# Optimization experiments

Measured on AMD Instinct MI355X. Metric: run time of the kernel, lower is better.

The kernel has to match this reference:

```python
import jax, jax.numpy as jnp
import numpy as np

EPS = 1e-5  # BatchNorm eps; BN applied in eval mode with running_mean=0, running_var=1


def conv1x1(x, w, b=None):
    # x: [B,C,H,W], w: [O,C] -> [B,O,H,W]
    y = jnp.einsum('bchw,oc->bohw', x, w)
    if b is not None:
        y = y + b[None, :, None, None]
    return y


def bn_eval(x, gamma, beta):
    # running_mean=0, running_var=1
    scale = gamma / jnp.sqrt(1.0 + EPS)
    return x * scale[None, :, None, None] + beta[None, :, None, None]


def glnl_forward(x, mask, wt_nl, bt_nl, wp_nl, bp_nl, wt_l, bt_l, wp_l, bp_l,
                 wg_nl, bg_nl, wg_l, bg_l, wW, bW, gW, betaW, wWl, gWl, betaWl):
    B, C, H, W = x.shape
    I = wt_nl.shape[0]
    N = H * W

    # non-local branch score [B,N,N]
    th_nl = conv1x1(x, wt_nl, bt_nl).reshape(B, I, N)
    ph_nl = conv1x1(x, wp_nl, bp_nl).reshape(B, I, N)
    score_nl = jax.nn.softmax(jnp.einsum('bin,bim->bnm', th_nl, ph_nl), axis=-1)

    # local branch: mask-gated projections, score [B,N,N]
    m = mask.reshape(B, 1, N)
    th_l = conv1x1(x, wt_l, bt_l).reshape(B, I, N) * m
    ph_l = conv1x1(x, wp_l, bp_l).reshape(B, I, N) * m
    score_l = jax.nn.softmax(jnp.einsum('bin,bim->bnm', th_l, ph_l), axis=-1)

    # value projections [B,I,N]
    g_nl = conv1x1(x, wg_nl, bg_nl).reshape(B, I, N)
    g_l = conv1x1(x, wg_l, bg_l).reshape(B, I, N)

    # attention aggregation -> [B,I,H,W]
    y_nl = jnp.einsum('bnm,bim->bin', score_nl, g_nl).reshape(B, I, H, W)
    y_l = jnp.einsum('bnm,bim->bin', score_l, g_l).reshape(B, I, H, W)

    # W_local: conv1x1 (no bias) -> ReLU -> BN
    y_l = bn_eval(jax.nn.relu(conv1x1(y_l, wWl)), gWl, betaWl)

    y = y_nl + y_l
    # W: conv1x1 -> ReLU -> BN, then residual
    W_y = bn_eval(jax.nn.relu(conv1x1(y, wW, bW)), gW, betaW)
    return W_y + x


def setup_inputs() -> dict:
    key = jax.random.key(0)
    ks = jax.random.split(key, 20)
    B, C, I, H, W = 4, 128, 64, 64, 64
    s = 0.02
    inp = {
        'x': jax.random.normal(ks[0], (B, C, H, W), jnp.float32),
        'mask': (jax.random.uniform(ks[1], (B, 1, H, W)) > 0.5).astype(jnp.float32),
        'wt_nl': jax.random.normal(ks[2], (I, C)) * s, 'bt_nl': jnp.zeros((I,)),
        'wp_nl': jax.random.normal(ks[3], (I, C)) * s, 'bp_nl': jnp.zeros((I,)),
        'wt_l': jax.random.normal(ks[4], (I, C)) * s, 'bt_l': jnp.zeros((I,)),
        'wp_l': jax.random.normal(ks[5], (I, C)) * s, 'bp_l': jnp.zeros((I,)),
        'wg_nl': jax.random.normal(ks[6], (I, C)) * s, 'bg_nl': jnp.zeros((I,)),
        'wg_l': jax.random.normal(ks[7], (I, C)) * s, 'bg_l': jnp.zeros((I,)),
        'wW': jax.random.normal(ks[8], (C, I)) * s, 'bW': jnp.zeros((C,)),
        'gW': jnp.ones((C,)), 'betaW': jnp.zeros((C,)),
        'wWl': jax.random.normal(ks[9], (I, I)) * s,
        'gWl': jnp.ones((I,)), 'betaWl': jnp.zeros((I,)),
    }
    return inp


def reference(x, mask, wt_nl, bt_nl, wp_nl, bp_nl, wt_l, bt_l, wp_l, bp_l,
              wg_nl, bg_nl, wg_l, bg_l, wW, bW, gW, betaW, wWl, gWl, betaWl):
    return glnl_forward(x, mask, wt_nl, bt_nl, wp_nl, bp_nl, wt_l, bt_l, wp_l, bp_l,
                        wg_nl, bg_nl, wg_l, bg_l, wW, bW, gW, betaW, wWl, gWl, betaWl)
```

## Files before the change

### kernel.cpp

```cpp
#include <hip/hip_runtime.h>

typedef unsigned short u16;
typedef __attribute__((ext_vector_type(8))) short short8;
typedef __attribute__((ext_vector_type(4))) float floatx4;

#define MFMA16(a, b, c) __builtin_amdgcn_mfma_f32_16x16x32_bf16((a), (b), (c), 0, 0, 0)

#define SZ_P ((size_t)4 * 64 * 4096)

__device__ __forceinline__ float bf2f(u16 u) {
    union { unsigned int i; float f; } v; v.i = ((unsigned int)u) << 16; return v.f;
}
__device__ __forceinline__ u16 f2bf(float f) {
    union { float f; unsigned int i; } v; v.f = f;
    unsigned int r = v.i + 0x7fffu + ((v.i >> 16) & 1u);
    return (u16)(r >> 16);
}
__device__ __forceinline__ short8 pack8(const float* __restrict__ p) {
    short8 r;
#pragma unroll
    for (int j = 0; j < 8; ++j) r[j] = (short)f2bf(p[j]);
    return r;
}
__device__ __forceinline__ unsigned int pk2(float a, float b) {
    union { float f; unsigned int u; } x, y; x.f = a; y.f = b;
    return (x.u >> 16) | (y.u & 0xffff0000u);
}

__global__ __launch_bounds__(256) void k_proj(
    const float* __restrict__ x, const float* __restrict__ mask,
    const float* __restrict__ wq0, const float* __restrict__ bq0,
    const float* __restrict__ wk0, const float* __restrict__ bk0,
    const float* __restrict__ wv0, const float* __restrict__ bv0,
    const float* __restrict__ wq1, const float* __restrict__ bq1,
    const float* __restrict__ wk1, const float* __restrict__ bk1,
    const float* __restrict__ wv1, const float* __restrict__ bv1,
    u16* __restrict__ q0, u16* __restrict__ k0, u16* __restrict__ v0,
    u16* __restrict__ q1, u16* __restrict__ k1, u16* __restrict__ v1)
{
    __shared__ __align__(16) u16 xt_s[64 * 136];
    const int n0 = blockIdx.x * 64, b = blockIdx.y, br = blockIdx.z;
    const float* wq = br ? wq1 : wq0;  const float* bq = br ? bq1 : bq0;
    const float* wk = br ? wk1 : wk0;  const float* bk = br ? bk1 : bk0;
    const float* wv = br ? wv1 : wv0;  const float* bv = br ? bv1 : bv0;
    u16* q = br ? q1 : q0;  u16* k = br ? k1 : k0;  u16* v = br ? v1 : v0;

    const int t = threadIdx.x, w = t >> 6, lane = t & 63;
    const int quad = lane >> 4, l15 = lane & 15;
    const float* xb = x + ((size_t)b << 19);

    for (int idx = t; idx < 8192; idx += 256) {
        const int c = idx >> 6, n = idx & 63;
        xt_s[n * 136 + c] = f2bf(xb[((size_t)c << 12) + n0 + n]);
    }
    __syncthreads();

    short8 ax[4];
#pragma unroll
    for (int cc = 0; cc < 4; ++cc)
        ax[cc] = *(const short8*)&xt_s[(w * 16 + l15) * 136 + quad * 8 + cc * 32];

    float mv[4] = {1.f, 1.f, 1.f, 1.f};
    if (br) {
#pragma unroll
        for (int r = 0; r < 4; ++r)
            mv[r] = mask[((size_t)b << 12) + n0 + w * 16 + quad * 4 + r];
    }

#pragma unroll
    for (int qk = 0; qk < 2; ++qk) {
        const float* wsel = qk ? wk : wq;
        const float* bb = qk ? bk : bq;
        u16* o = qk ? k : q;
#pragma unroll
        for (int ns = 0; ns < 4; ++ns) {
            floatx4 acc = {0.f, 0.f, 0.f, 0.f};
            const float* wp = wsel + (ns * 16 + l15) * 128 + quad * 8;
#pragma unroll
            for (int cc = 0; cc < 4; ++cc)
                acc = MFMA16(ax[cc], pack8(wp + cc * 32), acc);
            const float bias_i = bb[ns * 16 + l15];
#pragma unroll
            for (int r = 0; r < 4; ++r) {
                const float val = (acc[r] + bias_i) * mv[r];
                o[((size_t)b << 18) + (size_t)(n0 + w * 16 + quad * 4 + r) * 64
                  + ns * 16 + l15] = f2bf(val);
            }
        }
    }

    short8 aw[4];
#pragma unroll
    for (int cc = 0; cc < 4; ++cc)
        aw[cc] = pack8(wv + (w * 16 + l15) * 128 + quad * 8 + cc * 32);
    float bvr[4];
#pragma unroll
    for (int r = 0; r < 4; ++r) bvr[r] = bv[w * 16 + quad * 4 + r];
#pragma unroll
    for (int ns = 0; ns < 4; ++ns) {
        floatx4 acc = {0.f, 0.f, 0.f, 0.f};
#pragma unroll
        for (int cc = 0; cc < 4; ++cc)
            acc = MFMA16(aw[cc],
                *(const short8*)&xt_s[(ns * 16 + l15) * 136 + quad * 8 + cc * 32], acc);
#pragma unroll
        for (int r = 0; r < 4; ++r) {
            v[((size_t)b << 18) + ((size_t)(w * 16 + quad * 4 + r) << 12)
              + n0 + ns * 16 + l15] = f2bf(acc[r] + bvr[r]);
        }
    }
}

__global__ __launch_bounds__(256) void k_flash(
    const u16* __restrict__ Q0, const u16* __restrict__ K0,
    const u16* __restrict__ V0,
    const u16* __restrict__ Q1, const u16* __restrict__ K1,
    const u16* __restrict__ V1,
    u16* __restrict__ num, float* __restrict__ den)
{
    __shared__ __align__(16) u16 kt_s[2][64 * 72];
    __shared__ __align__(16) u16 vt_s[2][64 * 72];
    __shared__ __align__(16) u16 p_s[4 * 32 * 72];

    const int flat = blockIdx.x;
    const int g = flat & 15, tile = flat >> 4;
    const int b = g >> 2, z = g & 3;
    const int br = z >> 1, sp = z & 1;
    const int qb = tile * 128;
    const size_t base = ((size_t)b << 18);
    const u16* Q = (br ? Q1 : Q0) + base;
    const u16* K = (br ? K1 : K0) + base;
    const u16* V = (br ? V1 : V0) + base;
    u16* numo = num + (size_t)z * SZ_P + base;
    float* deno = den + z * 16384 + b * 4096;

    const int t = threadIdx.x, w = t >> 6, lane = t & 63;
    const int quad = lane >> 4, l15 = lane & 15;
    const int pw = w * 32 * 72;

    const int r0 = t >> 3, r1 = (t + 256) >> 3, cg8 = (t & 7) * 8;
    const u16* Kp0 = K + (size_t)r0 * 64 + cg8;
    const u16* Kp1 = K + (size_t)r1 * 64 + cg8;
    const u16* Vp0 = V + ((size_t)r0 << 12) + cg8;
    const u16* Vp1 = V + ((size_t)r1 << 12) + cg8;
    const int lk0 = r0 * 72 + cg8, lk1 = r1 * 72 + cg8;

    short8 aq[2][2];
#pragma unroll
    for (int t2 = 0; t2 < 2; ++t2)
#pragma unroll
        for (int s = 0; s < 2; ++s)
            aq[t2][s] = *(const short8*)(Q + (size_t)(qb + w * 32 + t2 * 16 + l15) * 64
                                         + s * 32 + quad * 8);

    floatx4 oacc[4][2];
#pragma unroll
    for (int it = 0; it < 4; ++it)
#pragma unroll
        for (int t2 = 0; t2 < 2; ++t2) oacc[it][t2] = (floatx4){0.f, 0.f, 0.f, 0.f};
    float dacc[2] = {0.f, 0.f};

    const int roff = tile & 31;
    const int m_beg = sp * 2048;

    {
        const int m0 = m_beg + (roff << 6);
        *(short8*)&kt_s[0][lk0] = *(const short8*)(Kp0 + (size_t)m0 * 64);
        *(short8*)&kt_s[0][lk1] = *(const short8*)(Kp1 + (size_t)m0 * 64);
        *(short8*)&vt_s[0][lk0] = *(const short8*)(Vp0 + m0);
        *(short8*)&vt_s[0][lk1] = *(const short8*)(Vp1 + m0);
    }

    for (int j = 0; j < 32; ++j) {
        const int cur = j & 1;
        const int mn = m_beg + (((roff + j + 1) & 31) << 6);
        short8 pk0v = *(const short8*)(Kp0 + (size_t)mn * 64);
        short8 pk1v = *(const short8*)(Kp1 + (size_t)mn * 64);
        short8 pv0v = *(const short8*)(Vp0 + mn);
        short8 pv1v = *(const short8*)(Vp1 + mn);
        __syncthreads();

#pragma unroll
        for (int mt = 0; mt < 4; ++mt) {
            const u16* kp = &kt_s[cur][(mt * 16 + l15) * 72 + quad * 8];
            const short8 ka0 = *(const short8*)kp;
            const short8 ka1 = *(const short8*)(kp + 32);
#pragma unroll
            for (int t2 = 0; t2 < 2; ++t2) {
                floatx4 acc = {0.f, 0.f, 0.f, 0.f};
                acc = MFMA16(ka0, aq[t2][0], acc);
                acc = MFMA16(ka1, aq[t2][1], acc);
                const float e0 = __expf(acc[0]), e1 = __expf(acc[1]);
                const float e2 = __expf(acc[2]), e3 = __expf(acc[3]);
                dacc[t2] += (e0 + e1) + (e2 + e3);
                *(uint2*)&p_s[pw + (t2 * 16 + l15) * 72 + mt * 16 + quad * 4] =
                    make_uint2(pk2(e0, e1), pk2(e2, e3));
            }
        }

        short8 pb2[2][2];
#pragma unroll
        for (int t2 = 0; t2 < 2; ++t2)
#pragma unroll
            for (int s = 0; s < 2; ++s)
                pb2[t2][s] = *(const short8*)&p_s[pw + (t2 * 16 + l15) * 72 + s * 32 + quad * 8];
#pragma unroll
        for (int it = 0; it < 4; ++it) {
            const u16* vp = &vt_s[cur][(it * 16 + l15) * 72 + quad * 8];
            const short8 va0 = *(const short8*)vp;
            const short8 va1 = *(const short8*)(vp + 32);
#pragma unroll
            for (int t2 = 0; t2 < 2; ++t2) {
                oacc[it][t2] = MFMA16(va0, pb2[t2][0], oacc[it][t2]);
                oacc[it][t2] = MFMA16(va1, pb2[t2][1], oacc[it][t2]);
            }
        }

        *(short8*)&kt_s[cur ^ 1][lk0] = pk0v;
        *(short8*)&kt_s[cur ^ 1][lk1] = pk1v;
        *(short8*)&vt_s[cur ^ 1][lk0] = pv0v;
        *(short8*)&vt_s[cur ^ 1][lk1] = pv1v;
    }

#pragma unroll
    for (int t2 = 0; t2 < 2; ++t2) {
        float d = dacc[t2];
        d += __shfl_xor(d, 16, 64);
        d += __shfl_xor(d, 32, 64);
        if (quad == 0) deno[qb + w * 32 + t2 * 16 + l15] = d;
    }

#pragma unroll
    for (int it = 0; it < 4; ++it)
#pragma unroll
        for (int t2 = 0; t2 < 2; ++t2) {
            *(uint2*)&p_s[pw + (t2 * 16 + l15) * 72 + it * 16 + quad * 4] =
                make_uint2(pk2(oacc[it][t2][0], oacc[it][t2][1]),
                           pk2(oacc[it][t2][2], oacc[it][t2][3]));
        }
    __syncthreads();
#pragma unroll
    for (int ch = t; ch < 1024; ch += 256) {
        const int row = ch >> 3, cg = ch & 7;
        *(short8*)(numo + (size_t)(qb + row) * 64 + cg * 8) =
            *(const short8*)&p_s[(row >> 5) * 2304 + (row & 31) * 72 + cg * 8];
    }
}

__global__ __launch_bounds__(256) void k_epi(
    const u16* __restrict__ num, const float* __restrict__ den,
    const float* __restrict__ wWl, const float* __restrict__ gWl,
    const float* __restrict__ betaWl,
    const float* __restrict__ wW, const float* __restrict__ bW,
    const float* __restrict__ gW, const float* __restrict__ betaW,
    const float* __restrict__ x, float* __restrict__ out)
{
    __shared__ __align__(16) u16 yl_s[16 * 72];
    __shared__ __align__(16) u16 ynl_s[16 * 72];
    __shared__ __align__(16) u16 yy_s[16 * 72];
    const int b = blockIdx.y, n0 = blockIdx.x * 16;
    const int t = threadIdx.x, w = t >> 6, lane = t & 63;
    const int quad = lane >> 4, l15 = lane & 15;
    const size_t ybase = ((size_t)b << 18) + (size_t)n0 * 64;

    if (t < 128) {
        const int row = t >> 3, cg = t & 7;
        const float dn = den[b * 4096 + n0 + row] + den[16384 + b * 4096 + n0 + row];
        const float dl = den[32768 + b * 4096 + n0 + row] + den[49152 + b * 4096 + n0 + row];
        const float inl = 1.0f / dn, ilo = 1.0f / dl;
        const short8 a0 = *(const short8*)(num + ybase + row * 64 + cg * 8);
        const short8 a1 = *(const short8*)(num + SZ_P + ybase + row * 64 + cg * 8);
        const short8 c0 = *(const short8*)(num + 2 * SZ_P + ybase + row * 64 + cg * 8);
        const short8 c1 = *(const short8*)(num + 3 * SZ_P + ybase + row * 64 + cg * 8);
        short8 ynl8, yl8;
#pragma unroll
        for (int j = 0; j < 8; ++j) {
            ynl8[j] = (short)f2bf((bf2f((u16)a0[j]) + bf2f((u16)a1[j])) * inl);
            yl8[j]  = (short)f2bf((bf2f((u16)c0[j]) + bf2f((u16)c1[j])) * ilo);
        }
        *(short8*)&ynl_s[row * 72 + cg * 8] = ynl8;
        *(short8*)&yl_s[row * 72 + cg * 8] = yl8;
    }
    __syncthreads();
    const float rsq = rsqrtf(1.0f + 1e-5f);

    {
        const short8 a0 = pack8(wWl + (w * 16 + l15) * 64 + quad * 8);
        const short8 a1 = pack8(wWl + (w * 16 + l15) * 64 + 32 + quad * 8);
        float sc[4], bt[4];
#pragma unroll
        for (int r = 0; r < 4; ++r) {
            const int io = w * 16 + quad * 4 + r;
            sc[r] = gWl[io] * rsq;
            bt[r] = betaWl[io];
        }
        floatx4 acc = {0.f, 0.f, 0.f, 0.f};
        const u16* bp_ = &yl_s[l15 * 72 + quad * 8];
        acc = MFMA16(a0, *(const short8*)bp_, acc);
        acc = MFMA16(a1, *(const short8*)(bp_ + 32), acc);
#pragma unroll
        for (int r = 0; r < 4; ++r) {
            const int io = w * 16 + quad * 4 + r;
            float val = fmaxf(acc[r], 0.f) * sc[r] + bt[r];
            val += bf2f(ynl_s[l15 * 72 + io]);
            yy_s[l15 * 72 + io] = f2bf(val);
        }
    }
    __syncthreads();

#pragma unroll
    for (int rb = 0; rb < 2; ++rb) {
        const int c0 = rb * 64 + w * 16;
        const short8 a0 = pack8(wW + (c0 + l15) * 64 + quad * 8);
        const short8 a1 = pack8(wW + (c0 + l15) * 64 + 32 + quad * 8);
        float bs[4], sc[4], bt[4];
#pragma unroll
        for (int r = 0; r < 4; ++r) {
            const int c = c0 + quad * 4 + r;
            bs[r] = bW[c];
            sc[r] = gW[c] * rsq;
            bt[r] = betaW[c];
        }
        floatx4 acc = {0.f, 0.f, 0.f, 0.f};
        const u16* bp_ = &yy_s[l15 * 72 + quad * 8];
        acc = MFMA16(a0, *(const short8*)bp_, acc);
        acc = MFMA16(a1, *(const short8*)(bp_ + 32), acc);
#pragma unroll
        for (int r = 0; r < 4; ++r) {
            const int c = c0 + quad * 4 + r;
            float val = fmaxf(acc[r] + bs[r], 0.f) * sc[r] + bt[r];
            const size_t xi = ((size_t)b << 19) + ((size_t)c << 12) + n0 + l15;
            out[xi] = val + x[xi];
        }
    }
}

extern "C" void kernel_launch(void* const* d_in, const int* in_sizes, int n_in,
                              void* d_out, int out_size, void* d_ws, size_t ws_size,
                              hipStream_t stream) {
    const float* x      = (const float*)d_in[0];
    const float* mask   = (const float*)d_in[1];
    const float* wt_nl  = (const float*)d_in[2];  const float* bt_nl = (const float*)d_in[3];
    const float* wp_nl  = (const float*)d_in[4];  const float* bp_nl = (const float*)d_in[5];
    const float* wt_l   = (const float*)d_in[6];  const float* bt_l  = (const float*)d_in[7];
    const float* wp_l   = (const float*)d_in[8];  const float* bp_l  = (const float*)d_in[9];
    const float* wg_nl  = (const float*)d_in[10]; const float* bg_nl = (const float*)d_in[11];
    const float* wg_l   = (const float*)d_in[12]; const float* bg_l  = (const float*)d_in[13];
    const float* wW     = (const float*)d_in[14]; const float* bW    = (const float*)d_in[15];
    const float* gW     = (const float*)d_in[16]; const float* betaW = (const float*)d_in[17];
    const float* wWl    = (const float*)d_in[18]; const float* gWl   = (const float*)d_in[19];
    const float* betaWl = (const float*)d_in[20];

    u16* ws  = (u16*)d_ws;
    u16* q0  = ws;
    u16* k0  = q0 + SZ_P;
    u16* v0  = k0 + SZ_P;
    u16* q1  = v0 + SZ_P;
    u16* k1  = q1 + SZ_P;
    u16* v1  = k1 + SZ_P;
    u16* num = v1 + SZ_P;
    float* den = (float*)(num + 4 * SZ_P);

    k_proj<<<dim3(64, 4, 2), 256, 0, stream>>>(x, mask,
        wt_nl, bt_nl, wp_nl, bp_nl, wg_nl, bg_nl,
        wt_l,  bt_l,  wp_l,  bp_l,  wg_l,  bg_l,
        q0, k0, v0, q1, k1, v1);
    k_flash<<<dim3(512), 256, 0, stream>>>(q0, k0, v0, q1, k1, v1, num, den);
    k_epi<<<dim3(256, 4), 256, 0, stream>>>(num, den, wWl, gWl, betaWl,
                                            wW, bW, gW, betaW, x, (float*)d_out);
}
```

Measured before the change: 189.7 us.

## Split key range four ways with 512-thread flash blocks and exp2 softmax

The flash kernel now uses 512-thread blocks covering 256 query rows each. The key dimension is split into four partitions instead of two, and each iteration loads one K/V chunk per thread. The epilogue sums four partial numerators and denominators per branch, and the workspace grows to hold eight partial buffers. Q is pre-scaled by log2(e) in the projection kernel so the inner loop can use exp2f instead of __expf. This trades extra partial-sum traffic and workspace for shorter per-block loops and more warps per block sharing each K/V tile.

```diff
diff --git a/kernel.cpp b/kernel.cpp
--- a/kernel.cpp
+++ b/kernel.cpp
@@ -5,6 +5,7 @@
 typedef __attribute__((ext_vector_type(4))) float floatx4;
 
 #define MFMA16(a, b, c) __builtin_amdgcn_mfma_f32_16x16x32_bf16((a), (b), (c), 0, 0, 0)
+#define LOG2E 1.44269504088896340736f
 
 #define SZ_P ((size_t)4 * 64 * 4096)
 
@@ -72,6 +73,7 @@
         const float* wsel = qk ? wk : wq;
         const float* bb = qk ? bk : bq;
         u16* o = qk ? k : q;
+        const float qscale = qk ? 1.0f : LOG2E;
 #pragma unroll
         for (int ns = 0; ns < 4; ++ns) {
             floatx4 acc = {0.f, 0.f, 0.f, 0.f};
@@ -82,7 +84,7 @@
             const float bias_i = bb[ns * 16 + l15];
 #pragma unroll
             for (int r = 0; r < 4; ++r) {
-                const float val = (acc[r] + bias_i) * mv[r];
+                const float val = (acc[r] + bias_i) * mv[r] * qscale;
                 o[((size_t)b << 18) + (size_t)(n0 + w * 16 + quad * 4 + r) * 64
                   + ns * 16 + l15] = f2bf(val);
             }
@@ -111,7 +113,7 @@
     }
 }
 
-__global__ __launch_bounds__(256) void k_flash(
+__global__ __launch_bounds__(512, 4) void k_flash(
     const u16* __restrict__ Q0, const u16* __restrict__ K0,
     const u16* __restrict__ V0,
     const u16* __restrict__ Q1, const u16* __restrict__ K1,
@@ -120,13 +122,13 @@
 {
     __shared__ __align__(16) u16 kt_s[2][64 * 72];
     __shared__ __align__(16) u16 vt_s[2][64 * 72];
-    __shared__ __align__(16) u16 p_s[4 * 32 * 72];
+    __shared__ __align__(16) u16 p_s[8 * 32 * 72];
 
     const int flat = blockIdx.x;
-    const int g = flat & 15, tile = flat >> 4;
-    const int b = g >> 2, z = g & 3;
-    const int br = z >> 1, sp = z & 1;
-    const int qb = tile * 128;
+    const int g = flat & 31, tile = flat >> 5;
+    const int b = g >> 3, br = (g >> 2) & 1, sp = g & 3;
+    const int z = br * 4 + sp;
+    const int qb = tile * 256;
     const size_t base = ((size_t)b << 18);
     const u16* Q = (br ? Q1 : Q0) + base;
     const u16* K = (br ? K1 : K0) + base;
@@ -138,12 +140,10 @@
     const int quad = lane >> 4, l15 = lane & 15;
     const int pw = w * 32 * 72;
 
-    const int r0 = t >> 3, r1 = (t + 256) >> 3, cg8 = (t & 7) * 8;
+    const int r0 = t >> 3, cg8 = (t & 7) * 8;
     const u16* Kp0 = K + (size_t)r0 * 64 + cg8;
-    const u16* Kp1 = K + (size_t)r1 * 64 + cg8;
     const u16* Vp0 = V + ((size_t)r0 << 12) + cg8;
-    const u16* Vp1 = V + ((size_t)r1 << 12) + cg8;
-    const int lk0 = r0 * 72 + cg8, lk1 = r1 * 72 + cg8;
+    const int lk0 = r0 * 72 + cg8;
 
     short8 aq[2][2];
 #pragma unroll
@@ -160,24 +160,20 @@
         for (int t2 = 0; t2 < 2; ++t2) oacc[it][t2] = (floatx4){0.f, 0.f, 0.f, 0.f};
     float dacc[2] = {0.f, 0.f};
 
-    const int roff = tile & 31;
-    const int m_beg = sp * 2048;
+    const int roff = tile & 15;
+    const int m_beg = sp * 1024;
 
     {
         const int m0 = m_beg + (roff << 6);
         *(short8*)&kt_s[0][lk0] = *(const short8*)(Kp0 + (size_t)m0 * 64);
-        *(short8*)&kt_s[0][lk1] = *(const short8*)(Kp1 + (size_t)m0 * 64);
         *(short8*)&vt_s[0][lk0] = *(const short8*)(Vp0 + m0);
-        *(short8*)&vt_s[0][lk1] = *(const short8*)(Vp1 + m0);
-    }
-
-    for (int j = 0; j < 32; ++j) {
+    }
+
+    for (int j = 0; j < 16; ++j) {
         const int cur = j & 1;
-        const int mn = m_beg + (((roff + j + 1) & 31) << 6);
-        short8 pk0v = *(const short8*)(Kp0 + (size_t)mn * 64);
-        short8 pk1v = *(const short8*)(Kp1 + (size_t)mn * 64);
-        short8 pv0v = *(const short8*)(Vp0 + mn);
-        short8 pv1v = *(const short8*)(Vp1 + mn);
+        const int mn = m_beg + (((roff + j + 1) & 15) << 6);
+        short8 pkv = *(const short8*)(Kp0 + (size_t)mn * 64);
+        short8 pvv = *(const short8*)(Vp0 + mn);
         __syncthreads();
 
 #pragma unroll
@@ -190,8 +186,8 @@
                 floatx4 acc = {0.f, 0.f, 0.f, 0.f};
                 acc = MFMA16(ka0, aq[t2][0], acc);
                 acc = MFMA16(ka1, aq[t2][1], acc);
-                const float e0 = __expf(acc[0]), e1 = __expf(acc[1]);
-                const float e2 = __expf(acc[2]), e3 = __expf(acc[3]);
+                const float e0 = exp2f(acc[0]), e1 = exp2f(acc[1]);
+                const float e2 = exp2f(acc[2]), e3 = exp2f(acc[3]);
                 dacc[t2] += (e0 + e1) + (e2 + e3);
                 *(uint2*)&p_s[pw + (t2 * 16 + l15) * 72 + mt * 16 + quad * 4] =
                     make_uint2(pk2(e0, e1), pk2(e2, e3));
@@ -216,10 +212,8 @@
             }
         }
 
-        *(short8*)&kt_s[cur ^ 1][lk0] = pk0v;
-        *(short8*)&kt_s[cur ^ 1][lk1] = pk1v;
-        *(short8*)&vt_s[cur ^ 1][lk0] = pv0v;
-        *(short8*)&vt_s[cur ^ 1][lk1] = pv1v;
+        *(short8*)&kt_s[cur ^ 1][lk0] = pkv;
+        *(short8*)&vt_s[cur ^ 1][lk0] = pvv;
     }
 
 #pragma unroll
@@ -240,7 +234,7 @@
         }
     __syncthreads();
 #pragma unroll
-    for (int ch = t; ch < 1024; ch += 256) {
+    for (int ch = t; ch < 2048; ch += 512) {
         const int row = ch >> 3, cg = ch & 7;
         *(short8*)(numo + (size_t)(qb + row) * 64 + cg * 8) =
             *(const short8*)&p_s[(row >> 5) * 2304 + (row & 31) * 72 + cg * 8];
@@ -265,18 +259,29 @@
 
     if (t < 128) {
         const int row = t >> 3, cg = t & 7;
-        const float dn = den[b * 4096 + n0 + row] + den[16384 + b * 4096 + n0 + row];
-        const float dl = den[32768 + b * 4096 + n0 + row] + den[49152 + b * 4096 + n0 + row];
+        float dn = 0.f, dl = 0.f;
+#pragma unroll
+        for (int sp = 0; sp < 4; ++sp) {
+            dn += den[sp * 16384 + b * 4096 + n0 + row];
+            dl += den[(4 + sp) * 16384 + b * 4096 + n0 + row];
+        }
         const float inl = 1.0f / dn, ilo = 1.0f / dl;
-        const short8 a0 = *(const short8*)(num + ybase + row * 64 + cg * 8);
-        const short8 a1 = *(const short8*)(num + SZ_P + ybase + row * 64 + cg * 8);
-        const short8 c0 = *(const short8*)(num + 2 * SZ_P + ybase + row * 64 + cg * 8);
-        const short8 c1 = *(const short8*)(num + 3 * SZ_P + ybase + row * 64 + cg * 8);
+        float an[8] = {0, 0, 0, 0, 0, 0, 0, 0}, al[8] = {0, 0, 0, 0, 0, 0, 0, 0};
+#pragma unroll
+        for (int sp = 0; sp < 4; ++sp) {
+            const short8 vn = *(const short8*)(num + (size_t)sp * SZ_P + ybase + row * 64 + cg * 8);
+            const short8 vl = *(const short8*)(num + (size_t)(4 + sp) * SZ_P + ybase + row * 64 + cg * 8);
+#pragma unroll
+            for (int j = 0; j < 8; ++j) {
+                an[j] += bf2f((u16)vn[j]);
+                al[j] += bf2f((u16)vl[j]);
+            }
+        }
         short8 ynl8, yl8;
 #pragma unroll
         for (int j = 0; j < 8; ++j) {
-            ynl8[j] = (short)f2bf((bf2f((u16)a0[j]) + bf2f((u16)a1[j])) * inl);
-            yl8[j]  = (short)f2bf((bf2f((u16)c0[j]) + bf2f((u16)c1[j])) * ilo);
+            ynl8[j] = (short)f2bf(an[j] * inl);
+            yl8[j]  = (short)f2bf(al[j] * ilo);
         }
         *(short8*)&ynl_s[row * 72 + cg * 8] = ynl8;
         *(short8*)&yl_s[row * 72 + cg * 8] = yl8;
@@ -359,13 +364,13 @@
     u16* k1  = q1 + SZ_P;
     u16* v1  = k1 + SZ_P;
     u16* num = v1 + SZ_P;
-    float* den = (float*)(num + 4 * SZ_P);
+    float* den = (float*)(num + 8 * SZ_P);
 
     k_proj<<<dim3(64, 4, 2), 256, 0, stream>>>(x, mask,
         wt_nl, bt_nl, wp_nl, bp_nl, wg_nl, bg_nl,
         wt_l,  bt_l,  wp_l,  bp_l,  wg_l,  bg_l,
         q0, k0, v0, q1, k1, v1);
-    k_flash<<<dim3(512), 256, 0, stream>>>(q0, k0, v0, q1, k1, v1, num, den);
+    k_flash<<<dim3(512), 512, 0, stream>>>(q0, k0, v0, q1, k1, v1, num, den);
     k_epi<<<dim3(256, 4), 256, 0, stream>>>(num, den, wWl, gWl, betaWl,
                                             wW, bW, gW, betaW, x, (float*)d_out);
 }
```

Result: faster. 184.9 us (-2.5%).
